# Kernel optimization log

Measured on AMD Instinct MI355X. Metric: run time of the kernel, lower is better.

## Reference

```python
import jax, jax.numpy as jnp
import numpy as np

EPS = 1e-08
N_NODES = 100000
E_HALF = 3200000  # directed edges before symmetrization


def setup_inputs() -> dict:
    key = jax.random.key(0)
    k1, k2, k3 = jax.random.split(key, 3)
    pos = jax.random.normal(k1, (N_NODES, 3), dtype=jnp.float32)
    phi = jax.random.normal(k2, (N_NODES,), dtype=jnp.float32)
    e = jax.random.randint(k3, (2, E_HALF), 0, N_NODES, dtype=jnp.int32)
    # symmetrize (the torch module calls to_undirected); build undirected edge list
    edge_index = jnp.concatenate([e, e[::-1]], axis=1)  # (2, 2*E_HALF)
    return {"pos": pos, "phi": phi, "edge_index": edge_index}


def reference(pos, phi, edge_index):
    # pos: (N, 3), phi: (N,), edge_index: (2, E) already undirected
    n = pos.shape[0]
    row, col = edge_index[0], edge_index[1]
    dx = pos[col] - pos[row]                      # (E, 3)
    dphi = phi[col] - phi[row]                    # (E,)
    w = 1.0 / (jnp.linalg.norm(dx, axis=1) + EPS) ** 2  # (E,)
    outer = dx[:, :, None] * dx[:, None, :]      # (E, 3, 3)
    A = jax.ops.segment_sum(w[:, None, None] * outer, row, num_segments=n)  # (N,3,3)
    b = jax.ops.segment_sum((w * dphi)[:, None] * dx, row, num_segments=n)  # (N,3)
    A_reg = A + EPS * jnp.eye(3, dtype=pos.dtype)[None, :, :]
    grad_phi = jnp.linalg.solve(A_reg, b[..., None])[..., 0]  # (N,3)
    return grad_phi
```

## Files before the change

### kernel.cpp

```cpp
#include <hip/hip_runtime.h>
#include <hip/hip_bf16.h>
#include <math.h>

#define LSQ_EPS 1e-8f
#define BUCKET_BITS 7
#define BUCKET_SIZE 128
#define NB_MAX 800
#define CAP 8960
#define SCAT_BLOCKS 1024
#define STAGE_CAP 6272
#define VEC_ITERS 4

__device__ __forceinline__ int hget(const unsigned int* hp, int b) {
    return (int)((hp[b >> 1] >> ((b & 1) * 16)) & 0xFFFFu);
}
__device__ __forceinline__ unsigned int hinc_rank(unsigned int* hp, int b) {
    unsigned int o = atomicAdd(&hp[b >> 1], 1u << ((b & 1) * 16));
    return (o >> ((b & 1) * 16)) & 0xFFFFu;
}

__global__ __launch_bounds__(256, 5) void lsq_scatter_sorted(
    const float* __restrict__ pos, const float* __restrict__ phi,
    const int* __restrict__ eidx, int E, int N, int NB,
    float4* __restrict__ pp4,
    unsigned int* __restrict__ region, unsigned int* __restrict__ meta)
{
    __shared__ unsigned int staged[STAGE_CAP];
    __shared__ unsigned int histp[NB_MAX / 2];
    __shared__ unsigned short sstart16[NB_MAX];

    const int tid = threadIdx.x;
    const int E2 = E >> 1;

    for (int i = blockIdx.x * 256 + tid; i < N; i += SCAT_BLOCKS * 256)
        pp4[i] = make_float4(pos[3 * i + 0], pos[3 * i + 1], pos[3 * i + 2], phi[i]);

    int chunk = (E2 + SCAT_BLOCKS - 1) / SCAT_BLOCKS;
    chunk = (chunk + 3) & ~3;
    const int start = blockIdx.x * chunk;
    const int end = min(start + chunk, E2);
    if (start >= E2) return;

    for (int t = tid; t < NB_MAX / 2; t += 256) histp[t] = 0;
    __syncthreads();

    const int nvec = (end - start) & ~3;
    unsigned int rkA[VEC_ITERS][4];
    int4 rA[VEC_ITERS], cA[VEC_ITERS];
#pragma unroll
    for (int k = 0; k < VEC_ITERS; ++k) {
        int e = start + (tid << 2) + (k << 10);
        if (e < start + nvec) {
            int4 r = *(const int4*)(eidx + e);
            int4 c = *(const int4*)(eidx + E + e);
            rA[k] = r;
            cA[k] = c;
            rkA[k][0] = hinc_rank(histp, r.x >> BUCKET_BITS) |
                        (hinc_rank(histp, c.x >> BUCKET_BITS) << 16);
            rkA[k][1] = hinc_rank(histp, r.y >> BUCKET_BITS) |
                        (hinc_rank(histp, c.y >> BUCKET_BITS) << 16);
            rkA[k][2] = hinc_rank(histp, r.z >> BUCKET_BITS) |
                        (hinc_rank(histp, c.z >> BUCKET_BITS) << 16);
            rkA[k][3] = hinc_rank(histp, r.w >> BUCKET_BITS) |
                        (hinc_rank(histp, c.w >> BUCKET_BITS) << 16);
        }
    }
    unsigned int rkT = 0;
    int trow = 0, tcol = 0;
    const int tcnt = (end - start) - nvec;
    if (tid < tcnt) {
        int e = start + nvec + tid;
        trow = eidx[e];
        tcol = eidx[E + e];
        rkT = hinc_rank(histp, trow >> BUCKET_BITS) |
              (hinc_rank(histp, tcol >> BUCKET_BITS) << 16);
    }
    __syncthreads();

    if (tid < 64) {
        int carry = 0;
        for (int bi = 0; bi < NB; bi += 64) {
            int b = bi + tid;
            int c = (b < NB) ? hget(histp, b) : 0;
            int x = c;
#pragma unroll
            for (int d = 1; d < 64; d <<= 1) {
                int y = __shfl_up(x, d, 64);
                if (tid >= d) x += y;
            }
            if (b < NB) sstart16[b] = (unsigned short)(carry + x - c);
            carry += __shfl(x, 63, 64);
        }
    }
    __syncthreads();

    {
        unsigned int* mrow = meta + (size_t)blockIdx.x * NB;
        for (int b = tid; b < NB; b += 256)
            mrow[b] = ((unsigned int)sstart16[b] << 16) | (unsigned int)hget(histp, b);
    }

#pragma unroll
    for (int k = 0; k < VEC_ITERS; ++k) {
        int e = start + (tid << 2) + (k << 10);
        if (e < start + nvec) {
            int rr[4] = {rA[k].x, rA[k].y, rA[k].z, rA[k].w};
            int cc[4] = {cA[k].x, cA[k].y, cA[k].z, cA[k].w};
#pragma unroll
            for (int q = 0; q < 4; ++q) {
                int b1 = rr[q] >> BUCKET_BITS;
                int s1 = (int)sstart16[b1] + (int)(rkA[k][q] & 0xFFFFu);
                staged[s1] = ((unsigned int)(rr[q] & (BUCKET_SIZE - 1)) << 17) | (unsigned int)cc[q];
                int b2 = cc[q] >> BUCKET_BITS;
                int s2 = (int)sstart16[b2] + (int)(rkA[k][q] >> 16);
                staged[s2] = ((unsigned int)(cc[q] & (BUCKET_SIZE - 1)) << 17) | (unsigned int)rr[q];
            }
        }
    }
    if (tid < tcnt) {
        int b1 = trow >> BUCKET_BITS;
        staged[(int)sstart16[b1] + (int)(rkT & 0xFFFFu)] =
            ((unsigned int)(trow & (BUCKET_SIZE - 1)) << 17) | (unsigned int)tcol;
        int b2 = tcol >> BUCKET_BITS;
        staged[(int)sstart16[b2] + (int)(rkT >> 16)] =
            ((unsigned int)(tcol & (BUCKET_SIZE - 1)) << 17) | (unsigned int)trow;
    }
    __syncthreads();

    {
        const int fill4 = (2 * (end - start)) >> 2;
        uint4* dst4 = (uint4*)(region + (size_t)blockIdx.x * (2 * chunk));
        const uint4* src4 = (const uint4*)staged;
        for (int i = tid; i < fill4; i += 256)
            dst4[i] = src4[i];
    }
}

#define LSQ_ACC(qv)                                                            \
    {                                                                          \
        float dx = (qv).x - me.x;                                              \
        float dy = (qv).y - me.y;                                              \
        float dz = (qv).z - me.z;                                              \
        float dphi = (qv).w - me.w;                                            \
        float nn = sqrtf(dx * dx + dy * dy + dz * dz) + LSQ_EPS;               \
        float w = 1.0f / (nn * nn);                                            \
        float wd = w * dphi;                                                   \
        a00 += w * dx * dx; a01 += w * dx * dy; a02 += w * dx * dz;            \
        a11 += w * dy * dy; a12 += w * dy * dz; a22 += w * dz * dz;            \
        bb0 += wd * dx;     bb1 += wd * dy;     bb2 += wd * dz;                \
    }

__global__ __launch_bounds__(512, 4) void lsq_bucket_reduce(
    const float4* __restrict__ pp4,
    const unsigned int* __restrict__ region, const unsigned int* __restrict__ meta,
    float* __restrict__ out, int N, int E, int NB)
{
    __shared__ unsigned int buf1[CAP];
    __shared__ unsigned int sorted32[CAP];
    __shared__ unsigned short mcnt[SCAT_BLOCKS];
    __shared__ unsigned short msrt[SCAT_BLOCKS];
    __shared__ unsigned short pblk[SCAT_BLOCKS];
    __shared__ int cnt[BUCKET_SIZE];
    __shared__ int startx[BUCKET_SIZE];
    __shared__ int tot_s;

    const int b = blockIdx.x;
    const int tid = threadIdx.x;
    const int node_base = b << BUCKET_BITS;
    const int E2 = E >> 1;
    int chunk = (E2 + SCAT_BLOCKS - 1) / SCAT_BLOCKS;
    chunk = (chunk + 3) & ~3;
    const int nblk = min(SCAT_BLOCKS, (E2 + chunk - 1) / chunk);
    const int BSTRIDE = 2 * chunk;

    if (tid < BUCKET_SIZE) cnt[tid] = 0;

    for (int r = tid; r < SCAT_BLOCKS; r += 512) {
        unsigned int m = (r < nblk) ? meta[(size_t)r * NB + b] : 0u;
        mcnt[r] = (unsigned short)(m & 0xFFFFu);
        msrt[r] = (unsigned short)(m >> 16);
    }
    __syncthreads();

    if (tid < 64) {
        int carry = 0;
        for (int base = 0; base < SCAT_BLOCKS; base += 64) {
            int c = (int)mcnt[base + tid];
            int x = c;
#pragma unroll
            for (int d = 1; d < 64; d <<= 1) {
                int y = __shfl_up(x, d, 64);
                if (tid >= d) x += y;
            }
            pblk[base + tid] = (unsigned short)min(carry + x - c, 65535);
            carry += __shfl(x, 63, 64);
        }
        if (tid == 0) tot_s = carry;
    }
    __syncthreads();
    const int total = min(tot_s, CAP);

    {
        const int wv = tid >> 6, ln = tid & 63;
        const int grp = ln >> 3, sub = ln & 7;
        for (int r = wv * 8 + grp; r < SCAT_BLOCKS; r += 64) {
            int len = (int)mcnt[r];
            if (len == 0) continue;
            int dst0 = (int)pblk[r];
            int kmax = min(len, CAP - dst0);
            const unsigned int* srcp = region + (size_t)r * BSTRIDE + (int)msrt[r];
            for (int j = sub; j < kmax; j += 8) {
                unsigned int p = srcp[j];
                unsigned int rk = (unsigned int)atomicAdd(&cnt[(p >> 17) & 0x7F], 1);
                buf1[dst0 + j] = (p & 0x00FFFFFFu) | (rk << 24);
            }
        }
    }
    __syncthreads();

    if (tid < 64) {
        int c0 = cnt[tid];
        int c1 = cnt[tid + 64];
        int x0 = c0, x1 = c1;
#pragma unroll
        for (int d = 1; d < 64; d <<= 1) {
            int y0 = __shfl_up(x0, d, 64);
            int y1 = __shfl_up(x1, d, 64);
            if (tid >= d) { x0 += y0; x1 += y1; }
        }
        int tot0 = __shfl(x0, 63, 64);
        startx[tid] = x0 - c0;
        startx[tid + 64] = tot0 + x1 - c1;
    }
    __syncthreads();

    for (int i = tid; i < total; i += 512) {
        unsigned int p = buf1[i];
        sorted32[startx[(p >> 17) & 0x7Fu] + (int)(p >> 24)] = p & 0x1FFFFu;
    }
    __syncthreads();

    const int n = tid >> 2;
    const int qid = tid & 3;
    int node = node_base + n;
    float4 me = pp4[node < N ? node : 0];
    const int s = startx[n];
    const int cN = cnt[n];
    int lo = s + (cN * qid) / 4;
    const int hi = s + (cN * (qid + 1)) / 4;

    float a00 = 0, a01 = 0, a02 = 0, a11 = 0, a12 = 0, a22 = 0;
    float bb0 = 0, bb1 = 0, bb2 = 0;

    int i = lo;
    float4 q0, q1, q2, q3;
    bool have = (i + 3 < hi);
    if (have) {
        int c0 = (int)sorted32[i];
        int c1 = (int)sorted32[i + 1];
        int c2 = (int)sorted32[i + 2];
        int c3 = (int)sorted32[i + 3];
        q0 = pp4[c0]; q1 = pp4[c1]; q2 = pp4[c2]; q3 = pp4[c3];
    }
    while (have) {
        const int j = i + 4;
        const bool nhave = (j + 3 < hi);
        float4 p0, p1, p2, p3;
        if (nhave) {
            int c0 = (int)sorted32[j];
            int c1 = (int)sorted32[j + 1];
            int c2 = (int)sorted32[j + 2];
            int c3 = (int)sorted32[j + 3];
            p0 = pp4[c0]; p1 = pp4[c1]; p2 = pp4[c2]; p3 = pp4[c3];
        }
        LSQ_ACC(q0); LSQ_ACC(q1); LSQ_ACC(q2); LSQ_ACC(q3);
        q0 = p0; q1 = p1; q2 = p2; q3 = p3;
        i = j;
        have = nhave;
    }
    for (; i < hi; ++i) {
        int c0 = (int)sorted32[i];
        float4 qt = pp4[c0];
        LSQ_ACC(qt);
    }

    a00 += __shfl_down(a00, 1); a01 += __shfl_down(a01, 1);
    a02 += __shfl_down(a02, 1); a11 += __shfl_down(a11, 1);
    a12 += __shfl_down(a12, 1); a22 += __shfl_down(a22, 1);
    bb0 += __shfl_down(bb0, 1); bb1 += __shfl_down(bb1, 1);
    bb2 += __shfl_down(bb2, 1);
    a00 += __shfl_down(a00, 2); a01 += __shfl_down(a01, 2);
    a02 += __shfl_down(a02, 2); a11 += __shfl_down(a11, 2);
    a12 += __shfl_down(a12, 2); a22 += __shfl_down(a22, 2);
    bb0 += __shfl_down(bb0, 2); bb1 += __shfl_down(bb1, 2);
    bb2 += __shfl_down(bb2, 2);

    if (qid == 0 && node < N) {
        double a00d = (double)a00 + 1e-8;
        double a01d = (double)a01;
        double a02d = (double)a02;
        double a11d = (double)a11 + 1e-8;
        double a12d = (double)a12;
        double a22d = (double)a22 + 1e-8;
        double b0 = (double)bb0;
        double b1 = (double)bb1;
        double b2 = (double)bb2;

        double c00 = a11d * a22d - a12d * a12d;
        double c01 = a02d * a12d - a01d * a22d;
        double c02 = a01d * a12d - a02d * a11d;
        double c11 = a00d * a22d - a02d * a02d;
        double c12 = a01d * a02d - a00d * a12d;
        double c22 = a00d * a11d - a01d * a01d;

        double det = a00d * c00 + a01d * c01 + a02d * c02;
        double inv = 1.0 / det;

        out[node * 3 + 0] = (float)((c00 * b0 + c01 * b1 + c02 * b2) * inv);
        out[node * 3 + 1] = (float)((c01 * b0 + c11 * b1 + c12 * b2) * inv);
        out[node * 3 + 2] = (float)((c02 * b0 + c12 * b1 + c22 * b2) * inv);
    }
}

__global__ void lsq_edge_scatter(const float* __restrict__ pos,
                                 const float* __restrict__ phi,
                                 const int* __restrict__ eidx,
                                 float* __restrict__ acc,
                                 int E) {
    int e = blockIdx.x * blockDim.x + threadIdx.x;
    if (e >= E) return;
    int r = eidx[e];
    int c = eidx[E + e];
    float dx = pos[3 * c + 0] - pos[3 * r + 0];
    float dy = pos[3 * c + 1] - pos[3 * r + 1];
    float dz = pos[3 * c + 2] - pos[3 * r + 2];
    float dphi = phi[c] - phi[r];
    float n = sqrtf(dx * dx + dy * dy + dz * dz) + LSQ_EPS;
    float w = 1.0f / (n * n);
    float wd = w * dphi;
    float* a = acc + (size_t)r * 9;
    unsafeAtomicAdd(a + 0, w * dx * dx);
    unsafeAtomicAdd(a + 1, w * dx * dy);
    unsafeAtomicAdd(a + 2, w * dx * dz);
    unsafeAtomicAdd(a + 3, w * dy * dy);
    unsafeAtomicAdd(a + 4, w * dy * dz);
    unsafeAtomicAdd(a + 5, w * dz * dz);
    unsafeAtomicAdd(a + 6, wd * dx);
    unsafeAtomicAdd(a + 7, wd * dy);
    unsafeAtomicAdd(a + 8, wd * dz);
}

__global__ void lsq_solve3(const float* __restrict__ acc,
                           float* __restrict__ out,
                           int N) {
    int i = blockIdx.x * blockDim.x + threadIdx.x;
    if (i >= N) return;
    const float* a = acc + (size_t)i * 9;
    double a00 = (double)a[0] + 1e-8;
    double a01 = (double)a[1];
    double a02 = (double)a[2];
    double a11 = (double)a[3] + 1e-8;
    double a12 = (double)a[4];
    double a22 = (double)a[5] + 1e-8;
    double b0 = (double)a[6];
    double b1 = (double)a[7];
    double b2 = (double)a[8];
    double c00 = a11 * a22 - a12 * a12;
    double c01 = a02 * a12 - a01 * a22;
    double c02 = a01 * a12 - a02 * a11;
    double c11 = a00 * a22 - a02 * a02;
    double c12 = a01 * a02 - a00 * a12;
    double c22 = a00 * a11 - a01 * a01;
    double det = a00 * c00 + a01 * c01 + a02 * c02;
    double inv = 1.0 / det;
    out[3 * i + 0] = (float)((c00 * b0 + c01 * b1 + c02 * b2) * inv);
    out[3 * i + 1] = (float)((c01 * b0 + c11 * b1 + c12 * b2) * inv);
    out[3 * i + 2] = (float)((c02 * b0 + c12 * b1 + c22 * b2) * inv);
}

extern "C" void kernel_launch(void* const* d_in, const int* in_sizes, int n_in,
                              void* d_out, int out_size, void* d_ws, size_t ws_size,
                              hipStream_t stream) {
    const float* pos = (const float*)d_in[0];
    const float* phi = (const float*)d_in[1];
    const int* eidx = (const int*)d_in[2];
    float* out = (float*)d_out;

    int N = in_sizes[0] / 3;
    int E = in_sizes[2] / 2;
    int NB = (N + BUCKET_SIZE - 1) >> BUCKET_BITS;

    int chunk = ((E / 2) + SCAT_BLOCKS - 1) / SCAT_BLOCKS;
    chunk = (chunk + 3) & ~3;
    bool stage_ok = (2 * chunk) <= STAGE_CAP;

    size_t region_bytes = (size_t)SCAT_BLOCKS * 2 * chunk * sizeof(unsigned int);
    size_t pp4_bytes = (size_t)N * sizeof(float4);
    size_t meta_bytes = (size_t)SCAT_BLOCKS * NB * sizeof(unsigned int);
    size_t need = region_bytes + pp4_bytes + meta_bytes;

    if (NB <= NB_MAX && ws_size >= need && (E & 3) == 0 && stage_ok) {
        unsigned int* region = (unsigned int*)d_ws;
        float4* pp4 = (float4*)((char*)d_ws + region_bytes);
        unsigned int* meta = (unsigned int*)((char*)d_ws + region_bytes + pp4_bytes);

        lsq_scatter_sorted<<<SCAT_BLOCKS, 256, 0, stream>>>(
            pos, phi, eidx, E, N, NB, pp4, region, meta);
        lsq_bucket_reduce<<<NB, 512, 0, stream>>>(pp4, region, meta, out, N, E, NB);
    } else {
        float* acc = (float*)d_ws;
        hipMemsetAsync(acc, 0, (size_t)N * 9 * sizeof(float), stream);
        int threads = 256;
        lsq_edge_scatter<<<(E + threads - 1) / threads, threads, 0, stream>>>(pos, phi, eidx, acc, E);
        lsq_solve3<<<(N + threads - 1) / threads, threads, 0, stream>>>(acc, out, N);
    }
}
```

Baseline: 171.2 us.

## Enlarge node buckets and replace staged two-step sort with count-then-scatter

Bucket size grows from 128 to 512 nodes, and the reduce kernel runs with 1024 threads, two threads per node. The old block-prefix plus staging buffer is replaced. A first pass over the region counts edges per local node, a prefix sum follows, and a second pass scatters directly into the sorted LDS array. This drops one LDS buffer and a scatter step, at the cost of reading region twice. The reduce grid shrinks to about 196 blocks, each using most of the LDS, which risks leaving CUs idle. The software-pipelined gather loop is also simplified to a plain unrolled loop.

Result: no change. 173.3 us (+1.2%).

```diff
diff --git a/kernel.cpp b/kernel.cpp
--- a/kernel.cpp
+++ b/kernel.cpp
@@ -3,10 +3,10 @@
 #include <math.h>
 
 #define LSQ_EPS 1e-8f
-#define BUCKET_BITS 7
-#define BUCKET_SIZE 128
-#define NB_MAX 800
-#define CAP 8960
+#define BUCKET_BITS 9
+#define BUCKET_SIZE 512
+#define NB_MAX 200
+#define CAP 34304
 #define SCAT_BLOCKS 1024
 #define STAGE_CAP 6272
 #define VEC_ITERS 4
@@ -94,11 +94,9 @@
     }
     __syncthreads();
 
-    {
-        unsigned int* mrow = meta + (size_t)blockIdx.x * NB;
-        for (int b = tid; b < NB; b += 256)
-            mrow[b] = ((unsigned int)sstart16[b] << 16) | (unsigned int)hget(histp, b);
-    }
+    if (tid < NB)
+        meta[(size_t)blockIdx.x * NB + tid] =
+            ((unsigned int)sstart16[tid] << 16) | (unsigned int)hget(histp, tid);
 
 #pragma unroll
     for (int k = 0; k < VEC_ITERS; ++k) {
@@ -150,19 +148,17 @@
         bb0 += wd * dx;     bb1 += wd * dy;     bb2 += wd * dz;                \
     }
 
-__global__ __launch_bounds__(512, 4) void lsq_bucket_reduce(
+__global__ __launch_bounds__(1024, 4) void lsq_bucket_reduce(
     const float4* __restrict__ pp4,
     const unsigned int* __restrict__ region, const unsigned int* __restrict__ meta,
     float* __restrict__ out, int N, int E, int NB)
 {
-    __shared__ unsigned int buf1[CAP];
     __shared__ unsigned int sorted32[CAP];
     __shared__ unsigned short mcnt[SCAT_BLOCKS];
     __shared__ unsigned short msrt[SCAT_BLOCKS];
-    __shared__ unsigned short pblk[SCAT_BLOCKS];
     __shared__ int cnt[BUCKET_SIZE];
+    __shared__ int cnt2[BUCKET_SIZE];
     __shared__ int startx[BUCKET_SIZE];
-    __shared__ int tot_s;
 
     const int b = blockIdx.x;
     const int tid = threadIdx.x;
@@ -173,115 +169,90 @@
     const int nblk = min(SCAT_BLOCKS, (E2 + chunk - 1) / chunk);
     const int BSTRIDE = 2 * chunk;
 
-    if (tid < BUCKET_SIZE) cnt[tid] = 0;
-
-    for (int r = tid; r < SCAT_BLOCKS; r += 512) {
-        unsigned int m = (r < nblk) ? meta[(size_t)r * NB + b] : 0u;
-        mcnt[r] = (unsigned short)(m & 0xFFFFu);
-        msrt[r] = (unsigned short)(m >> 16);
+    if (tid < BUCKET_SIZE) { cnt[tid] = 0; cnt2[tid] = 0; }
+
+    if (tid < SCAT_BLOCKS) {
+        unsigned int m = (tid < nblk) ? meta[(size_t)tid * NB + b] : 0u;
+        mcnt[tid] = (unsigned short)(m & 0xFFFFu);
+        msrt[tid] = (unsigned short)(m >> 16);
+    }
+    __syncthreads();
+
+    {
+        const int g = tid >> 5;
+        const int sub = tid & 31;
+        for (int r = g; r < nblk; r += 32) {
+            int len = (int)mcnt[r];
+            const unsigned int* srcp = region + (size_t)r * BSTRIDE + (int)msrt[r];
+            for (int j = sub; j < len; j += 32)
+                atomicAdd(&cnt[srcp[j] >> 17], 1);
+        }
     }
     __syncthreads();
 
     if (tid < 64) {
         int carry = 0;
-        for (int base = 0; base < SCAT_BLOCKS; base += 64) {
-            int c = (int)mcnt[base + tid];
+        for (int base = 0; base < BUCKET_SIZE; base += 64) {
+            int c = cnt[base + tid];
             int x = c;
 #pragma unroll
             for (int d = 1; d < 64; d <<= 1) {
                 int y = __shfl_up(x, d, 64);
                 if (tid >= d) x += y;
             }
-            pblk[base + tid] = (unsigned short)min(carry + x - c, 65535);
+            startx[base + tid] = carry + x - c;
             carry += __shfl(x, 63, 64);
         }
-        if (tid == 0) tot_s = carry;
-    }
-    __syncthreads();
-    const int total = min(tot_s, CAP);
+    }
+    __syncthreads();
 
     {
-        const int wv = tid >> 6, ln = tid & 63;
-        const int grp = ln >> 3, sub = ln & 7;
-        for (int r = wv * 8 + grp; r < SCAT_BLOCKS; r += 64) {
+        const int g = tid >> 5;
+        const int sub = tid & 31;
+        for (int r = g; r < nblk; r += 32) {
             int len = (int)mcnt[r];
-            if (len == 0) continue;
-            int dst0 = (int)pblk[r];
-            int kmax = min(len, CAP - dst0);
             const unsigned int* srcp = region + (size_t)r * BSTRIDE + (int)msrt[r];
-            for (int j = sub; j < kmax; j += 8) {
+            for (int j = sub; j < len; j += 32) {
                 unsigned int p = srcp[j];
-                unsigned int rk = (unsigned int)atomicAdd(&cnt[(p >> 17) & 0x7F], 1);
-                buf1[dst0 + j] = (p & 0x00FFFFFFu) | (rk << 24);
+                int nl = (int)(p >> 17);
+                int rk = atomicAdd(&cnt2[nl], 1);
+                int idx = startx[nl] + rk;
+                if (idx < CAP) sorted32[idx] = p & 0x1FFFFu;
             }
         }
     }
     __syncthreads();
 
-    if (tid < 64) {
-        int c0 = cnt[tid];
-        int c1 = cnt[tid + 64];
-        int x0 = c0, x1 = c1;
-#pragma unroll
-        for (int d = 1; d < 64; d <<= 1) {
-            int y0 = __shfl_up(x0, d, 64);
-            int y1 = __shfl_up(x1, d, 64);
-            if (tid >= d) { x0 += y0; x1 += y1; }
-        }
-        int tot0 = __shfl(x0, 63, 64);
-        startx[tid] = x0 - c0;
-        startx[tid + 64] = tot0 + x1 - c1;
-    }
-    __syncthreads();
-
-    for (int i = tid; i < total; i += 512) {
-        unsigned int p = buf1[i];
-        sorted32[startx[(p >> 17) & 0x7Fu] + (int)(p >> 24)] = p & 0x1FFFFu;
-    }
-    __syncthreads();
-
-    const int n = tid >> 2;
-    const int qid = tid & 3;
+    const int n = tid >> 1;
+    const int qid = tid & 1;
     int node = node_base + n;
     float4 me = pp4[node < N ? node : 0];
     const int s = startx[n];
     const int cN = cnt[n];
-    int lo = s + (cN * qid) / 4;
-    const int hi = s + (cN * (qid + 1)) / 4;
+    int lo = s + (cN * qid) / 2;
+    int hi = s + (cN * (qid + 1)) / 2;
+    if (hi > CAP) hi = CAP;
+    if (lo > CAP) lo = CAP;
 
     float a00 = 0, a01 = 0, a02 = 0, a11 = 0, a12 = 0, a22 = 0;
     float bb0 = 0, bb1 = 0, bb2 = 0;
 
     int i = lo;
-    float4 q0, q1, q2, q3;
-    bool have = (i + 3 < hi);
-    if (have) {
+    for (; i + 3 < hi; i += 4) {
         int c0 = (int)sorted32[i];
         int c1 = (int)sorted32[i + 1];
         int c2 = (int)sorted32[i + 2];
         int c3 = (int)sorted32[i + 3];
-        q0 = pp4[c0]; q1 = pp4[c1]; q2 = pp4[c2]; q3 = pp4[c3];
-    }
-    while (have) {
-        const int j = i + 4;
-        const bool nhave = (j + 3 < hi);
-        float4 p0, p1, p2, p3;
-        if (nhave) {
-            int c0 = (int)sorted32[j];
-            int c1 = (int)sorted32[j + 1];
-            int c2 = (int)sorted32[j + 2];
-            int c3 = (int)sorted32[j + 3];
-            p0 = pp4[c0]; p1 = pp4[c1]; p2 = pp4[c2]; p3 = pp4[c3];
-        }
+        float4 q0 = pp4[c0];
+        float4 q1 = pp4[c1];
+        float4 q2 = pp4[c2];
+        float4 q3 = pp4[c3];
         LSQ_ACC(q0); LSQ_ACC(q1); LSQ_ACC(q2); LSQ_ACC(q3);
-        q0 = p0; q1 = p1; q2 = p2; q3 = p3;
-        i = j;
-        have = nhave;
     }
     for (; i < hi; ++i) {
         int c0 = (int)sorted32[i];
-        float4 qt = pp4[c0];
-        LSQ_ACC(qt);
+        float4 q0 = pp4[c0];
+        LSQ_ACC(q0);
     }
 
     a00 += __shfl_down(a00, 1); a01 += __shfl_down(a01, 1);
@@ -289,11 +260,6 @@
     a12 += __shfl_down(a12, 1); a22 += __shfl_down(a22, 1);
     bb0 += __shfl_down(bb0, 1); bb1 += __shfl_down(bb1, 1);
     bb2 += __shfl_down(bb2, 1);
-    a00 += __shfl_down(a00, 2); a01 += __shfl_down(a01, 2);
-    a02 += __shfl_down(a02, 2); a11 += __shfl_down(a11, 2);
-    a12 += __shfl_down(a12, 2); a22 += __shfl_down(a22, 2);
-    bb0 += __shfl_down(bb0, 2); bb1 += __shfl_down(bb1, 2);
-    bb2 += __shfl_down(bb2, 2);
 
     if (qid == 0 && node < N) {
         double a00d = (double)a00 + 1e-8;
@@ -406,7 +372,7 @@
 
         lsq_scatter_sorted<<<SCAT_BLOCKS, 256, 0, stream>>>(
             pos, phi, eidx, E, N, NB, pp4, region, meta);
-        lsq_bucket_reduce<<<NB, 512, 0, stream>>>(pp4, region, meta, out, N, E, NB);
+        lsq_bucket_reduce<<<NB, 1024, 0, stream>>>(pp4, region, meta, out, N, E, NB);
     } else {
         float* acc = (float*)d_ws;
         hipMemsetAsync(acc, 0, (size_t)N * 9 * sizeof(float), stream);
```
